# Kernel tuning notes

Measured on AMD Instinct MI355X. Metric: run time of the kernel, lower is better.

Reference implementation:

```python
import jax, jax.numpy as jnp
import numpy as np

B, MAXLEN = 256, 10000
N_ATOMS, N_BONDS, N_ANG, N_TOR = 2000, 1999, 1998, 1997
NBT, NAT, NTT = 50, 100, 200
EPS = 1e-8


def setup_inputs() -> dict:
    rng = np.random.default_rng(0)
    feats = np.zeros((B, MAXLEN, 9), np.float32)
    # col 0: atom types
    feats[:, :N_ATOMS, 0] = rng.integers(0, 20, (B, N_ATOMS))
    # col 5: flattened coords [3*N]
    coords = (rng.standard_normal((B, N_ATOMS, 3)) * 2.0).astype(np.float32)
    feats[:, :3 * N_ATOMS, 5] = coords.reshape(B, -1)
    # col 6: bonds (i, j, type) along a chain
    i = np.arange(N_BONDS, dtype=np.float32)
    bonds = np.zeros((B, N_BONDS, 3), np.float32)
    bonds[..., 0] = i; bonds[..., 1] = i + 1
    bonds[..., 2] = rng.integers(0, NBT, (B, N_BONDS))
    feats[:, :3 * N_BONDS, 6] = bonds.reshape(B, -1)
    # col 7: angles (i, j, k, type)
    a = np.arange(N_ANG, dtype=np.float32)
    angs = np.zeros((B, N_ANG, 4), np.float32)
    angs[..., 0] = a; angs[..., 1] = a + 1; angs[..., 2] = a + 2
    angs[..., 3] = rng.integers(0, NAT, (B, N_ANG))
    feats[:, :4 * N_ANG, 7] = angs.reshape(B, -1)
    # col 8: torsions (i, j, k, l, type)
    t = np.arange(N_TOR, dtype=np.float32)
    tors = np.zeros((B, N_TOR, 5), np.float32)
    tors[..., 0] = t; tors[..., 1] = t + 1; tors[..., 2] = t + 2; tors[..., 3] = t + 3
    tors[..., 4] = rng.integers(0, NTT, (B, N_TOR))
    feats[:, :5 * N_TOR, 8] = tors.reshape(B, -1)
    # per-column valid lengths
    lengths = np.zeros((B, 9), np.int32)
    lengths[:, 0] = N_ATOMS
    lengths[:, 5] = 3 * N_ATOMS
    lengths[:, 6] = 3 * N_BONDS
    lengths[:, 7] = 4 * N_ANG
    lengths[:, 8] = 5 * N_TOR
    # learned params: (k, eq_value, multiplicity) per type row
    P = NBT + NAT + NTT
    opt = np.abs(rng.standard_normal((P, 3))).astype(np.float32)
    opt[:, 2] = rng.integers(1, 4, P).astype(np.float32)
    return {
        "features": jnp.asarray(feats),
        "lengths": jnp.asarray(lengths),
        "opt_pars": jnp.asarray(opt),
        "bond_type": jnp.arange(NBT, dtype=jnp.float32),
        "angle_type": jnp.arange(NAT, dtype=jnp.float32) + NBT,
        "tor_type": jnp.arange(NTT, dtype=jnp.float32) + NBT + NAT,
    }


def _gather(coords, idx):
    # coords [B,N,3], idx [B,M] -> [B,M,3]
    return jnp.take_along_axis(
        coords, jnp.broadcast_to(idx[..., None], idx.shape + (3,)), axis=1)


def _energy(features, lengths, opt_pars, bond_map, angle_map, tor_map):
    Bn = features.shape[0]
    coords = features[:, :3 * N_ATOMS, 5].reshape(Bn, N_ATOMS, 3)
    bonds = features[:, :3 * N_BONDS, 6].reshape(Bn, N_BONDS, 3).astype(jnp.int32)
    angs = features[:, :4 * N_ANG, 7].reshape(Bn, N_ANG, 4).astype(jnp.int32)
    tors = features[:, :5 * N_TOR, 8].reshape(Bn, N_TOR, 5).astype(jnp.int32)

    # ---- bonds: harmonic E = k * (r - r0)^2 ----
    ri, rj = _gather(coords, bonds[..., 0]), _gather(coords, bonds[..., 1])
    r = jnp.sqrt(jnp.sum((ri - rj) ** 2, -1) + EPS)          # [B,NB]
    pb = opt_pars[bond_map[bonds[..., 2]]]                   # [B,NB,3]
    eb = pb[..., 0] * (r - pb[..., 1]) ** 2
    mb = jnp.arange(N_BONDS)[None, :] < (lengths[:, 6:7] // 3)
    ebonds = jnp.sum(jnp.where(mb, eb, 0.0), -1)

    # ---- angles: harmonic E = k * (theta - theta0)^2 ----
    ai, aj, ak = (_gather(coords, angs[..., c]) for c in range(3))
    u, v = ai - aj, ak - aj
    cos = jnp.sum(u * v, -1) * jax.lax.rsqrt(
        (jnp.sum(u * u, -1) + EPS) * (jnp.sum(v * v, -1) + EPS))
    theta = jnp.arccos(jnp.clip(cos, -1.0 + 1e-6, 1.0 - 1e-6))
    pa = opt_pars[angle_map[angs[..., 3]]]
    ea = pa[..., 0] * (theta - pa[..., 1]) ** 2
    ma = jnp.arange(N_ANG)[None, :] < (lengths[:, 7:8] // 4)
    eangles = jnp.sum(jnp.where(ma, ea, 0.0), -1)

    # ---- torsions: E = k * (1 + cos(n*phi - phi0)) ----
    ti, tj, tk, tl = (_gather(coords, tors[..., c]) for c in range(4))
    b1, b2, b3 = tj - ti, tk - tj, tl - tk
    n1 = jnp.cross(b1, b2)
    n2 = jnp.cross(b2, b3)
    b2h = b2 * jax.lax.rsqrt(jnp.sum(b2 * b2, -1, keepdims=True) + EPS)
    m1 = jnp.cross(n1, b2h)
    phi = jnp.arctan2(jnp.sum(m1 * n2, -1), jnp.sum(n1 * n2, -1))
    pt = opt_pars[tor_map[tors[..., 4]]]
    et = pt[..., 0] * (1.0 + jnp.cos(pt[..., 2] * phi - pt[..., 1]))
    mt = jnp.arange(N_TOR)[None, :] < (lengths[:, 8:9] // 5)
    etors = jnp.sum(jnp.where(mt, et, 0.0), -1)

    return ebonds + eangles + etors                          # [B]


def reference(features, lengths, opt_pars, bond_type, angle_type, tor_type):
    return _energy(features, lengths, opt_pars,
                   bond_type.astype(jnp.int32),
                   angle_type.astype(jnp.int32),
                   tor_type.astype(jnp.int32))
```

## Files before the change

kernel.cpp:

```cpp
#include <hip/hip_runtime.h>


#define BS 256
#define NSLICE 8

constexpr int BATCH   = 256;
constexpr int MAXLEN  = 10000;
constexpr int NBT = 50, NAT = 100, NTT = 200;
constexpr float EPS = 1e-8f;

constexpr size_t OFF_CC   = 0;
constexpr size_t OFF_BC   = OFF_CC + (size_t)BATCH * 6000 * 4;
constexpr size_t OFF_AC   = OFF_BC + (size_t)BATCH * 6000 * 2;
constexpr size_t OFF_TC   = OFF_AC + (size_t)BATCH * 8000 * 2;
constexpr size_t OFF_PART = OFF_TC + (size_t)BATCH * 10000 * 2;

__global__ __launch_bounds__(256) void compact_kernel(
    const float* __restrict__ features,
    float* __restrict__ cc, unsigned short* __restrict__ bc,
    unsigned short* __restrict__ ac, unsigned short* __restrict__ tc)
{
    const unsigned NV = (unsigned)BATCH * 22500u;
    const float4* __restrict__ fv = (const float4*)features;
    const unsigned stride = gridDim.x * 256u;
    for (unsigned q = blockIdx.x * 256u + threadIdx.x; q < NV; q += stride) {
        float4 v = fv[q];
        unsigned b = q / 22500u;
        unsigned g = (q - b * 22500u) * 4u;
        float vals[4] = {v.x, v.y, v.z, v.w};
        #pragma unroll
        for (int e = 0; e < 4; ++e) {
            unsigned gg  = g + (unsigned)e;
            unsigned i   = gg / 9u;
            unsigned col = gg - 9u * i;
            float    val = vals[e];
            if (col == 5u)      { if (i < 6000u) cc[b * 6000u  + i] = val; }
            else if (col == 6u) { if (i < 5997u) bc[b * 6000u  + i] = (unsigned short)(int)val; }
            else if (col == 7u) { if (i < 7992u) ac[b * 8000u  + i] = (unsigned short)(int)val; }
            else if (col == 8u) { if (i < 9985u) tc[b * 10000u + i] = (unsigned short)(int)val; }
        }
    }
}

__global__ __launch_bounds__(BS) void energy_slice_kernel(
    const float* __restrict__ cc,
    const unsigned short* __restrict__ bc,
    const unsigned short* __restrict__ ac,
    const unsigned short* __restrict__ tc,
    const int*   __restrict__ lengths,
    const float* __restrict__ opt_pars,
    const float* __restrict__ bond_type,
    const float* __restrict__ angle_type,
    const float* __restrict__ tor_type,
    float*       __restrict__ part)
{
    __shared__ float sbp[3 * NBT];
    __shared__ float sap[3 * NAT];
    __shared__ float stp[3 * NTT];
    __shared__ float sw[BS / 64];

    const int blk = blockIdx.x;
    const int b   = blk >> 3;
    const int s   = blk & (NSLICE - 1);
    const int tid = threadIdx.x;

    for (int i = tid; i < NBT; i += BS) {
        int idx = (int)bond_type[i];
        sbp[3*i+0] = opt_pars[3*idx+0];
        sbp[3*i+1] = opt_pars[3*idx+1];
        sbp[3*i+2] = opt_pars[3*idx+2];
    }
    for (int i = tid; i < NAT; i += BS) {
        int idx = (int)angle_type[i];
        sap[3*i+0] = opt_pars[3*idx+0];
        sap[3*i+1] = opt_pars[3*idx+1];
        sap[3*i+2] = opt_pars[3*idx+2];
    }
    for (int i = tid; i < NTT; i += BS) {
        int idx = (int)tor_type[i];
        stp[3*i+0] = opt_pars[3*idx+0];
        stp[3*i+1] = opt_pars[3*idx+1];
        stp[3*i+2] = opt_pars[3*idx+2];
    }
    __syncthreads();

    const float*          c = cc + (size_t)b * 6000;
    const unsigned short* B_ = bc + (size_t)b * 6000;
    const unsigned short* A_ = ac + (size_t)b * 8000;
    const unsigned short* T_ = tc + (size_t)b * 10000;

    float acc = 0.0f;

    {
        const int nb = lengths[b * 9 + 6] / 3;
        const int t0 = (nb * s) / NSLICE, t1 = (nb * (s + 1)) / NSLICE;
        for (int t = t0 + tid; t < t1; t += BS) {
            int i  = B_[3*t+0];
            int j  = B_[3*t+1];
            int ty = B_[3*t+2];
            float dx = c[3*i+0] - c[3*j+0];
            float dy = c[3*i+1] - c[3*j+1];
            float dz = c[3*i+2] - c[3*j+2];
            float r  = sqrtf(dx*dx + dy*dy + dz*dz + EPS);
            float k  = sbp[3*ty+0];
            float d  = r - sbp[3*ty+1];
            acc += k * d * d;
        }
    }

    {
        const int na = lengths[b * 9 + 7] / 4;
        const int t0 = (na * s) / NSLICE, t1 = (na * (s + 1)) / NSLICE;
        for (int t = t0 + tid; t < t1; t += BS) {
            int i  = A_[4*t+0];
            int j  = A_[4*t+1];
            int k_ = A_[4*t+2];
            int ty = A_[4*t+3];
            float jx = c[3*j+0], jy = c[3*j+1], jz = c[3*j+2];
            float ux = c[3*i+0] - jx, uy = c[3*i+1] - jy, uz = c[3*i+2] - jz;
            float vx = c[3*k_+0] - jx, vy = c[3*k_+1] - jy, vz = c[3*k_+2] - jz;
            float uv = ux*vx + uy*vy + uz*vz;
            float uu = ux*ux + uy*uy + uz*uz;
            float vv = vx*vx + vy*vy + vz*vz;
            float cth = uv * rsqrtf((uu + EPS) * (vv + EPS));
            cth = fminf(fmaxf(cth, -1.0f + 1e-6f), 1.0f - 1e-6f);
            float theta = acosf(cth);
            float k  = sap[3*ty+0];
            float d  = theta - sap[3*ty+1];
            acc += k * d * d;
        }
    }

    {
        const int nt = lengths[b * 9 + 8] / 5;
        const int t0 = (nt * s) / NSLICE, t1 = (nt * (s + 1)) / NSLICE;
        for (int t = t0 + tid; t < t1; t += BS) {
            int i  = T_[5*t+0];
            int j  = T_[5*t+1];
            int k_ = T_[5*t+2];
            int l  = T_[5*t+3];
            int ty = T_[5*t+4];
            float ix = c[3*i+0],  iy = c[3*i+1],  iz = c[3*i+2];
            float jx = c[3*j+0],  jy = c[3*j+1],  jz = c[3*j+2];
            float kx = c[3*k_+0], ky = c[3*k_+1], kz = c[3*k_+2];
            float lx = c[3*l+0],  ly = c[3*l+1],  lz = c[3*l+2];
            float b1x = jx - ix, b1y = jy - iy, b1z = jz - iz;
            float b2x = kx - jx, b2y = ky - jy, b2z = kz - jz;
            float b3x = lx - kx, b3y = ly - ky, b3z = lz - kz;
            float n1x = b1y*b2z - b1z*b2y;
            float n1y = b1z*b2x - b1x*b2z;
            float n1z = b1x*b2y - b1y*b2x;
            float n2x = b2y*b3z - b2z*b3y;
            float n2y = b2z*b3x - b2x*b3z;
            float n2z = b2x*b3y - b2y*b3x;
            float inv = rsqrtf(b2x*b2x + b2y*b2y + b2z*b2z + EPS);
            float hx = b2x * inv, hy = b2y * inv, hz = b2z * inv;
            float m1x = n1y*hz - n1z*hy;
            float m1y = n1z*hx - n1x*hz;
            float m1z = n1x*hy - n1y*hx;
            float sy = m1x*n2x + m1y*n2y + m1z*n2z;
            float sx = n1x*n2x + n1y*n2y + n1z*n2z;
            float phi = atan2f(sy, sx);
            float k  = stp[3*ty+0];
            float p0 = stp[3*ty+1];
            float n  = stp[3*ty+2];
            acc += k * (1.0f + cosf(n * phi - p0));
        }
    }

    for (int off = 32; off > 0; off >>= 1)
        acc += __shfl_down(acc, off, 64);
    const int wave = tid >> 6, lane = tid & 63;
    if (lane == 0) sw[wave] = acc;
    __syncthreads();
    if (tid == 0) {
        float v = 0.0f;
        #pragma unroll
        for (int w = 0; w < BS / 64; ++w) v += sw[w];
        part[blk] = v;
    }
}

__global__ __launch_bounds__(256) void reduce_kernel(
    const float* __restrict__ part, float* __restrict__ out, int B)
{
    int b = blockIdx.x * 256 + threadIdx.x;
    if (b < B) {
        float v = 0.0f;
        #pragma unroll
        for (int i = 0; i < NSLICE; ++i) v += part[b * NSLICE + i];
        out[b] = v;
    }
}

extern "C" void kernel_launch(void* const* d_in, const int* in_sizes, int n_in,
                              void* d_out, int out_size, void* d_ws, size_t ws_size,
                              hipStream_t stream) {
    const float* features   = (const float*)d_in[0];
    const int*   lengths    = (const int*)  d_in[1];
    const float* opt_pars   = (const float*)d_in[2];
    const float* bond_type  = (const float*)d_in[3];
    const float* angle_type = (const float*)d_in[4];
    const float* tor_type   = (const float*)d_in[5];
    float* out = (float*)d_out;
    char*  ws  = (char*)d_ws;

    float*          cc   = (float*)(ws + OFF_CC);
    unsigned short* bc   = (unsigned short*)(ws + OFF_BC);
    unsigned short* ac   = (unsigned short*)(ws + OFF_AC);
    unsigned short* tc   = (unsigned short*)(ws + OFF_TC);
    float*          part = (float*)(ws + OFF_PART);

    const int B = out_size;

    compact_kernel<<<4096, 256, 0, stream>>>(features, cc, bc, ac, tc);
    energy_slice_kernel<<<B * NSLICE, BS, 0, stream>>>(
        cc, bc, ac, tc, lengths, opt_pars, bond_type, angle_type, tor_type, part);
    reduce_kernel<<<(B + 255) / 256, 256, 0, stream>>>(part, out, B);
}
```

Measured before the change: 166.3 us.

## Restructure compaction per row and use one 1024-thread block per batch

```diff
diff --git a/kernel.cpp b/kernel.cpp
--- a/kernel.cpp
+++ b/kernel.cpp
@@ -1,48 +1,42 @@
 #include <hip/hip_runtime.h>
 
 
-#define BS 256
-#define NSLICE 8
+#define CBS 256
+#define EBS 1024
 
-constexpr int BATCH   = 256;
-constexpr int MAXLEN  = 10000;
+constexpr int BATCH  = 256;
+constexpr int MAXLEN = 10000;
 constexpr int NBT = 50, NAT = 100, NTT = 200;
 constexpr float EPS = 1e-8f;
 
-constexpr size_t OFF_CC   = 0;
-constexpr size_t OFF_BC   = OFF_CC + (size_t)BATCH * 6000 * 4;
-constexpr size_t OFF_AC   = OFF_BC + (size_t)BATCH * 6000 * 2;
-constexpr size_t OFF_TC   = OFF_AC + (size_t)BATCH * 8000 * 2;
-constexpr size_t OFF_PART = OFF_TC + (size_t)BATCH * 10000 * 2;
+constexpr size_t OFF_CC = 0;
+constexpr size_t OFF_BC = OFF_CC + (size_t)BATCH * 6000 * 4;
+constexpr size_t OFF_AC = OFF_BC + (size_t)BATCH * 6000 * 2;
+constexpr size_t OFF_TC = OFF_AC + (size_t)BATCH * 8000 * 2;
 
-__global__ __launch_bounds__(256) void compact_kernel(
+__global__ __launch_bounds__(CBS) void compact_kernel(
     const float* __restrict__ features,
     float* __restrict__ cc, unsigned short* __restrict__ bc,
     unsigned short* __restrict__ ac, unsigned short* __restrict__ tc)
 {
-    const unsigned NV = (unsigned)BATCH * 22500u;
-    const float4* __restrict__ fv = (const float4*)features;
-    const unsigned stride = gridDim.x * 256u;
-    for (unsigned q = blockIdx.x * 256u + threadIdx.x; q < NV; q += stride) {
-        float4 v = fv[q];
-        unsigned b = q / 22500u;
-        unsigned g = (q - b * 22500u) * 4u;
-        float vals[4] = {v.x, v.y, v.z, v.w};
-        #pragma unroll
-        for (int e = 0; e < 4; ++e) {
-            unsigned gg  = g + (unsigned)e;
-            unsigned i   = gg / 9u;
-            unsigned col = gg - 9u * i;
-            float    val = vals[e];
-            if (col == 5u)      { if (i < 6000u) cc[b * 6000u  + i] = val; }
-            else if (col == 6u) { if (i < 5997u) bc[b * 6000u  + i] = (unsigned short)(int)val; }
-            else if (col == 7u) { if (i < 7992u) ac[b * 8000u  + i] = (unsigned short)(int)val; }
-            else if (col == 8u) { if (i < 9985u) tc[b * 10000u + i] = (unsigned short)(int)val; }
-        }
-    }
+    const unsigned gid = blockIdx.x * CBS + threadIdx.x;
+    const unsigned b   = gid / (unsigned)MAXLEN;
+    const unsigned i   = gid - b * (unsigned)MAXLEN;
+    if (b >= (unsigned)BATCH) return;
+
+    const float* __restrict__ row = features + (size_t)b * MAXLEN * 9 + 9u * i + 5u;
+    float vc = row[0];
+    float vb = row[1];
+    float va = row[2];
+    float vt = row[3];
+
+    if (i < 6000u) cc[b * 6000u  + i] = vc;
+    if (i < 5997u) bc[b * 6000u  + i] = (unsigned short)(int)vb;
+    if (i < 7992u) ac[b * 8000u  + i] = (unsigned short)(int)va;
+    if (i < 9985u) tc[b * 10000u + i] = (unsigned short)(int)vt;
 }
 
-__global__ __launch_bounds__(BS) void energy_slice_kernel(
+__global__ __launch_bounds__(EBS) void energy_kernel(
     const float* __restrict__ cc,
     const unsigned short* __restrict__ bc,
     const unsigned short* __restrict__ ac,
@@ -52,31 +46,29 @@
     const float* __restrict__ bond_type,
     const float* __restrict__ angle_type,
     const float* __restrict__ tor_type,
-    float*       __restrict__ part)
+    float*       __restrict__ out)
 {
     __shared__ float sbp[3 * NBT];
     __shared__ float sap[3 * NAT];
     __shared__ float stp[3 * NTT];
-    __shared__ float sw[BS / 64];
+    __shared__ float sw[EBS / 64];
 
-    const int blk = blockIdx.x;
-    const int b   = blk >> 3;
-    const int s   = blk & (NSLICE - 1);
+    const int b   = blockIdx.x;
     const int tid = threadIdx.x;
 
-    for (int i = tid; i < NBT; i += BS) {
+    for (int i = tid; i < NBT; i += EBS) {
         int idx = (int)bond_type[i];
         sbp[3*i+0] = opt_pars[3*idx+0];
         sbp[3*i+1] = opt_pars[3*idx+1];
         sbp[3*i+2] = opt_pars[3*idx+2];
     }
-    for (int i = tid; i < NAT; i += BS) {
+    for (int i = tid; i < NAT; i += EBS) {
         int idx = (int)angle_type[i];
         sap[3*i+0] = opt_pars[3*idx+0];
         sap[3*i+1] = opt_pars[3*idx+1];
         sap[3*i+2] = opt_pars[3*idx+2];
     }
-    for (int i = tid; i < NTT; i += BS) {
+    for (int i = tid; i < NTT; i += EBS) {
         int idx = (int)tor_type[i];
         stp[3*i+0] = opt_pars[3*idx+0];
         stp[3*i+1] = opt_pars[3*idx+1];
@@ -84,7 +76,7 @@
     }
     __syncthreads();
 
-    const float*          c = cc + (size_t)b * 6000;
+    const float*          c  = cc + (size_t)b * 6000;
     const unsigned short* B_ = bc + (size_t)b * 6000;
     const unsigned short* A_ = ac + (size_t)b * 8000;
     const unsigned short* T_ = tc + (size_t)b * 10000;
@@ -93,8 +85,7 @@
 
     {
         const int nb = lengths[b * 9 + 6] / 3;
-        const int t0 = (nb * s) / NSLICE, t1 = (nb * (s + 1)) / NSLICE;
-        for (int t = t0 + tid; t < t1; t += BS) {
+        for (int t = tid; t < nb; t += EBS) {
             int i  = B_[3*t+0];
             int j  = B_[3*t+1];
             int ty = B_[3*t+2];
@@ -110,8 +101,7 @@
 
     {
         const int na = lengths[b * 9 + 7] / 4;
-        const int t0 = (na * s) / NSLICE, t1 = (na * (s + 1)) / NSLICE;
-        for (int t = t0 + tid; t < t1; t += BS) {
+        for (int t = tid; t < na; t += EBS) {
             int i  = A_[4*t+0];
             int j  = A_[4*t+1];
             int k_ = A_[4*t+2];
@@ -133,8 +123,7 @@
 
     {
         const int nt = lengths[b * 9 + 8] / 5;
-        const int t0 = (nt * s) / NSLICE, t1 = (nt * (s + 1)) / NSLICE;
-        for (int t = t0 + tid; t < t1; t += BS) {
+        for (int t = tid; t < nt; t += EBS) {
             int i  = T_[5*t+0];
             int j  = T_[5*t+1];
             int k_ = T_[5*t+2];
@@ -176,19 +165,7 @@
     if (tid == 0) {
         float v = 0.0f;
         #pragma unroll
-        for (int w = 0; w < BS / 64; ++w) v += sw[w];
-        part[blk] = v;
-    }
-}
-
-__global__ __launch_bounds__(256) void reduce_kernel(
-    const float* __restrict__ part, float* __restrict__ out, int B)
-{
-    int b = blockIdx.x * 256 + threadIdx.x;
-    if (b < B) {
-        float v = 0.0f;
-        #pragma unroll
-        for (int i = 0; i < NSLICE; ++i) v += part[b * NSLICE + i];
+        for (int w = 0; w < EBS / 64; ++w) v += sw[w];
         out[b] = v;
     }
 }
@@ -205,16 +182,15 @@
     float* out = (float*)d_out;
     char*  ws  = (char*)d_ws;
 
-    float*          cc   = (float*)(ws + OFF_CC);
-    unsigned short* bc   = (unsigned short*)(ws + OFF_BC);
-    unsigned short* ac   = (unsigned short*)(ws + OFF_AC);
-    unsigned short* tc   = (unsigned short*)(ws + OFF_TC);
-    float*          part = (float*)(ws + OFF_PART);
+    float*          cc = (float*)(ws + OFF_CC);
+    unsigned short* bc = (unsigned short*)(ws + OFF_BC);
+    unsigned short* ac = (unsigned short*)(ws + OFF_AC);
+    unsigned short* tc = (unsigned short*)(ws + OFF_TC);
 
     const int B = out_size;
-
-    compact_kernel<<<4096, 256, 0, stream>>>(features, cc, bc, ac, tc);
-    energy_slice_kernel<<<B * NSLICE, BS, 0, stream>>>(
-        cc, bc, ac, tc, lengths, opt_pars, bond_type, angle_type, tor_type, part);
-    reduce_kernel<<<(B + 255) / 256, 256, 0, stream>>>(part, out, B);
+    const int rows = BATCH * MAXLEN;
+    compact_kernel<<<(rows + CBS - 1) / CBS, CBS, 0, stream>>>(
+        features, cc, bc, ac, tc);
+    energy_kernel<<<B, EBS, 0, stream>>>(
+        cc, bc, ac, tc, lengths, opt_pars, bond_type, angle_type, tor_type, out);
 }
```

New measurement: 153.4 us. 7.7% less time.
